# Kernel optimization log

Measured on AMD Instinct MI355X. Metric: run time of the kernel, lower is better.

The kernel has to match this reference:

```python
import jax, jax.numpy as jnp
import numpy as np

HEAD_NUM = 16
KEY_DIM = 64
EMBED = 1024
KV_OUT = HEAD_NUM * KEY_DIM  # 1024


def setup_inputs() -> dict:
    key = jax.random.key(0)
    ks = jax.random.split(key, 11)
    B, L, E = 2, 2048, EMBED
    scale = 0.02
    return {
        "query": jax.random.normal(ks[0], (B, L, E), jnp.float32),
        "key": jax.random.normal(ks[1], (B, L, E), jnp.float32),
        "value": jax.random.normal(ks[2], (B, L, E), jnp.float32),
        "W_Query": jax.random.normal(ks[3], (E, KV_OUT), jnp.float32) * scale,
        "W_Key": jax.random.normal(ks[4], (E, KV_OUT), jnp.float32) * scale,
        "W_Value": jax.random.normal(ks[5], (E, KV_OUT), jnp.float32) * scale,
        "W_Output": jax.random.normal(ks[6], (KV_OUT, E), jnp.float32) * scale,
        "B_Query": jnp.zeros((KV_OUT,), jnp.float32),
        "B_Key": jnp.zeros((KV_OUT,), jnp.float32),
        "B_Value": jnp.zeros((KV_OUT,), jnp.float32),
        "B_Output": jnp.zeros((E,), jnp.float32),
    }


def reference(query, key, value, W_Query, W_Key, W_Value, W_Output,
              B_Query, B_Key, B_Value, B_Output):
    B, Lq, E = query.shape
    Lk = key.shape[1]
    H, D = HEAD_NUM, KEY_DIM
    # QKV projections + bias
    q = query @ W_Query + B_Query            # [B, Lq, H*D]
    k = key @ W_Key + B_Key                  # [B, Lk, H*D]
    v = value @ W_Value + B_Value            # [B, Lk, H*D]
    # tf.split(axis=2) per head == reshape to [B, L, H, D]
    q = q.reshape(B, Lq, H, D)
    k = k.reshape(B, Lk, H, D)
    v = v.reshape(B, Lk, H, D)
    # scaled dot-product attention (no mask, dropout=0)
    scores = jnp.einsum("bqhd,bkhd->bhqk", q, k) / (D ** 0.5)
    probs = jax.nn.softmax(scores, axis=-1)
    out = jnp.einsum("bhqk,bkhd->bqhd", probs, v)  # [B, Lq, H, D]
    out = out.reshape(B, Lq, H * D)
    return out @ W_Output + B_Output
```

## Files before the change

### kernel.cpp

```cpp
#include <hip/hip_runtime.h>

using u16 = unsigned short;
using u32 = unsigned int;

typedef __attribute__((ext_vector_type(8))) short bf16x8;
typedef __attribute__((ext_vector_type(4))) float f32x4;
typedef __attribute__((ext_vector_type(4))) u32 u32x4;
typedef __attribute__((ext_vector_type(2))) u32 u32x2;
typedef __attribute__((ext_vector_type(4))) _Float16 f16x4;

#define MFMA_BF16_K32(a, b, c) __builtin_amdgcn_mfma_f32_16x16x32_bf16((a), (b), (c), 0, 0, 0)
#define MFMA_F16_K16(a, b, c) __builtin_amdgcn_mfma_f32_16x16x16f16((a), (b), (c), 0, 0, 0)

#define QSCALE 0.18033688011112042f

extern "C" __device__ float __ocml_native_exp2_f32(float);

__device__ __forceinline__ u16 f2bf(float f) {
  u32 u = __builtin_bit_cast(u32, f);
  return (u16)((u + 0x7fffu + ((u >> 16) & 1u)) >> 16);
}

__device__ __forceinline__ u32 pk_f16(float a, float b) {
  auto v = __builtin_amdgcn_cvt_pkrtz(a, b);
  return __builtin_bit_cast(u32, v);
}

__device__ __forceinline__ void load_lds16(const void* g, void* l) {
  __builtin_amdgcn_global_load_lds((__attribute__((address_space(1))) void*)g,
                                   (__attribute__((address_space(3))) void*)l,
                                   16, 0, 0);
}

__global__ __launch_bounds__(256) void cvt_all_kernel(
    const float* __restrict__ q, const float* __restrict__ k, const float* __restrict__ v,
    u16* __restrict__ oq, u16* __restrict__ ok, u16* __restrict__ ov,
    const float* __restrict__ w0, const float* __restrict__ w1,
    const float* __restrict__ w2, const float* __restrict__ w3,
    u16* __restrict__ d0, u16* __restrict__ d1,
    u16* __restrict__ d2, u16* __restrict__ d3) {
  const int id = blockIdx.x;
  const int tid = threadIdx.x;
  if (id < 6144) {
    const int z = id >> 11, bx = id & 2047;
    const float* s = z == 0 ? q : z == 1 ? k : v;
    u16* d = z == 0 ? oq : z == 1 ? ok : ov;
    int i = (bx * 256 + tid) * 8;
    f32x4 a = *(const f32x4*)(s + i);
    f32x4 b = *(const f32x4*)(s + i + 4);
    u32x4 o;
    o.x = (u32)f2bf(a.x) | ((u32)f2bf(a.y) << 16);
    o.y = (u32)f2bf(a.z) | ((u32)f2bf(a.w) << 16);
    o.z = (u32)f2bf(b.x) | ((u32)f2bf(b.y) << 16);
    o.w = (u32)f2bf(b.z) | ((u32)f2bf(b.w) << 16);
    *(u32x4*)(d + i) = o;
    return;
  }
  __shared__ float t[64][65];
  const int r0 = id - 6144;
  const int z = r0 >> 8, rr0 = r0 & 255;
  const int bx = rr0 & 15, by = rr0 >> 4;
  const float* src = z == 0 ? w0 : z == 1 ? w1 : z == 2 ? w2 : w3;
  u16* dst = z == 0 ? d0 : z == 1 ? d1 : z == 2 ? d2 : d3;
  const float scale = (z == 0) ? QSCALE : 1.0f;
  const int r = tid >> 4, c4 = (tid & 15) * 4;
#pragma unroll
  for (int i = 0; i < 4; ++i) {
    int row = r + i * 16;
    f32x4 vv = *(const f32x4*)(src + (by * 64 + row) * 1024 + bx * 64 + c4);
    t[row][c4 + 0] = vv.x;
    t[row][c4 + 1] = vv.y;
    t[row][c4 + 2] = vv.z;
    t[row][c4 + 3] = vv.w;
  }
  __syncthreads();
  const int rw = tid >> 2, cc = (tid & 3) * 16;
  alignas(16) u16 tmp[16];
#pragma unroll
  for (int j = 0; j < 16; ++j) tmp[j] = f2bf(t[cc + j][rw] * scale);
  u32x4* outp = (u32x4*)(dst + (bx * 64 + rw) * 1024 + by * 64 + cc);
  outp[0] = *(const u32x4*)&tmp[0];
  outp[1] = *(const u32x4*)&tmp[8];
}

__global__ __launch_bounds__(256) void gemm_qkv_kernel(
    const u16* __restrict__ x0, const u16* __restrict__ x1, const u16* __restrict__ x2,
    const u16* __restrict__ w0, const u16* __restrict__ w1, const u16* __restrict__ w2,
    const float* __restrict__ b0, const float* __restrict__ b1, const float* __restrict__ b2,
    u16* __restrict__ c0, u16* __restrict__ c1, u16* __restrict__ vt) {
  __shared__ u16 As[128 * 64];
  __shared__ u16 Bs[128 * 64];
  const int lid = blockIdx.x;
  const int xcd = lid & 7, rr = lid >> 3;
  const int nb = rr & 7, slot = rr >> 3;
  const int g = slot * 8 + xcd;
  const int z = g >> 5, m_idx = g & 31;
  const u16* A = z == 0 ? x0 : z == 1 ? x1 : x2;
  const u16* Bt = z == 0 ? w0 : z == 1 ? w1 : w2;
  const float* bias = z == 0 ? b0 : z == 1 ? b1 : b2;
  const float bscale = z == 0 ? QSCALE : 1.0f;
  const int tid = threadIdx.x;
  const int wave = tid >> 6, lane = tid & 63;
  const int l16 = lane & 15, quad = lane >> 4;
  const int l7 = l16 & 7;
  const int wm = wave >> 1, wn = wave & 1;
  const int m0 = m_idx * 128, n0 = nb * 128;

  f32x4 acc[4][4];
  const f32x4 zf = {0.f, 0.f, 0.f, 0.f};
#pragma unroll
  for (int i = 0; i < 4; ++i)
#pragma unroll
    for (int j = 0; j < 4; ++j) acc[i][j] = zf;

  for (int kb = 0; kb < 1024; kb += 64) {
#pragma unroll
    for (int t = 0; t < 4; ++t) {
      int c = wave * 256 + t * 64 + lane;
      int row = c >> 3, sc8 = (c & 7) ^ (row & 7);
      load_lds16(A + (m0 + row) * 1024 + kb + sc8 * 8, &As[(wave * 256 + t * 64) * 8]);
    }
#pragma unroll
    for (int t = 0; t < 4; ++t) {
      int c = wave * 256 + t * 64 + lane;
      int row = c >> 3, sc8 = (c & 7) ^ (row & 7);
      load_lds16(Bt + (n0 + row) * 1024 + kb + sc8 * 8, &Bs[(wave * 256 + t * 64) * 8]);
    }
    asm volatile("s_waitcnt vmcnt(0)" ::: "memory");
    __syncthreads();
#pragma unroll
    for (int ks = 0; ks < 2; ++ks) {
      const int sch = (ks * 4 + quad) ^ l7;
      bf16x8 af[4], bfv[4];
#pragma unroll
      for (int mt = 0; mt < 4; ++mt)
        af[mt] = *(const bf16x8*)&As[(wm * 64 + mt * 16 + l16) * 64 + sch * 8];
#pragma unroll
      for (int nt = 0; nt < 4; ++nt)
        bfv[nt] = *(const bf16x8*)&Bs[(wn * 64 + nt * 16 + l16) * 64 + sch * 8];
#pragma unroll
      for (int mt = 0; mt < 4; ++mt)
#pragma unroll
        for (int nt = 0; nt < 4; ++nt) acc[mt][nt] = MFMA_BF16_K32(af[mt], bfv[nt], acc[mt][nt]);
    }
    __syncthreads();
  }

  float bv[4];
#pragma unroll
  for (int nt = 0; nt < 4; ++nt) bv[nt] = bias[n0 + wn * 64 + nt * 16 + l16] * bscale;
  if (z != 2) {
    u16* C = z == 0 ? c0 : c1;
#pragma unroll
    for (int mt = 0; mt < 4; ++mt)
#pragma unroll
      for (int nt = 0; nt < 4; ++nt)
#pragma unroll
        for (int r = 0; r < 4; ++r) {
          int row = m0 + wm * 64 + mt * 16 + quad * 4 + r;
          int col = n0 + wn * 64 + nt * 16 + l16;
          C[row * 1024 + col] = f2bf(acc[mt][nt][r] + bv[nt]);
        }
  } else {
#pragma unroll
    for (int mt = 0; mt < 4; ++mt)
#pragma unroll
      for (int nt = 0; nt < 4; ++nt) {
        int kvb = m0 + wm * 64 + mt * 16 + quad * 4;
        int bb = kvb >> 11, kv = kvb & 2047;
        int col = n0 + wn * 64 + nt * 16 + l16;
        int h = col >> 6, dt = (col >> 4) & 3, ld = col & 15;
        int pair = bb * 16 + h;
        int kb2 = kv >> 7, chunk = (kv >> 4) & 7, qd = (kv >> 2) & 3;
        f16x4 hv;
#pragma unroll
        for (int r = 0; r < 4; ++r) hv[r] = (_Float16)(acc[mt][nt][r] + bv[nt]);
        u16* dst = vt + ((((pair * 16 + kb2) * 8 + chunk) * 4 + dt) * 256) + qd * 64 + ld * 4;
        *(f16x4*)dst = hv;
      }
  }
}

__global__ __launch_bounds__(256) void gemm_out_kernel(const u16* __restrict__ A,
                                                       const u16* __restrict__ Bt,
                                                       const float* __restrict__ bias,
                                                       float* __restrict__ C) {
  __shared__ u16 As[64 * 64];
  __shared__ u16 Bs[128 * 64];
  const int lid = blockIdx.x;
  const int xcd = lid & 7, rr = lid >> 3;
  const int nb = rr & 7, slot = rr >> 3;
  const int by = slot * 8 + xcd;
  const int tid = threadIdx.x;
  const int wave = tid >> 6, lane = tid & 63;
  const int l16 = lane & 15, quad = lane >> 4;
  const int l7 = l16 & 7;
  const int m0 = by * 64, n0 = nb * 128;

  f32x4 acc[4][2];
  const f32x4 zf = {0.f, 0.f, 0.f, 0.f};
#pragma unroll
  for (int i = 0; i < 4; ++i)
#pragma unroll
    for (int j = 0; j < 2; ++j) acc[i][j] = zf;

  for (int kb = 0; kb < 1024; kb += 64) {
#pragma unroll
    for (int t = 0; t < 2; ++t) {
      int c = wave * 128 + t * 64 + lane;
      int row = c >> 3, sc8 = (c & 7) ^ (row & 7);
      load_lds16(A + (m0 + row) * 1024 + kb + sc8 * 8, &As[(wave * 128 + t * 64) * 8]);
    }
#pragma unroll
    for (int t = 0; t < 4; ++t) {
      int c = wave * 256 + t * 64 + lane;
      int row = c >> 3, sc8 = (c & 7) ^ (row & 7);
      load_lds16(Bt + (n0 + row) * 1024 + kb + sc8 * 8, &Bs[(wave * 256 + t * 64) * 8]);
    }
    asm volatile("s_waitcnt vmcnt(0)" ::: "memory");
    __syncthreads();
#pragma unroll
    for (int ks = 0; ks < 2; ++ks) {
      const int sch = (ks * 4 + quad) ^ l7;
      bf16x8 af[4], bfv[2];
#pragma unroll
      for (int mt = 0; mt < 4; ++mt)
        af[mt] = *(const bf16x8*)&As[(mt * 16 + l16) * 64 + sch * 8];
#pragma unroll
      for (int nt = 0; nt < 2; ++nt)
        bfv[nt] = *(const bf16x8*)&Bs[(wave * 32 + nt * 16 + l16) * 64 + sch * 8];
#pragma unroll
      for (int mt = 0; mt < 4; ++mt)
#pragma unroll
        for (int nt = 0; nt < 2; ++nt) acc[mt][nt] = MFMA_BF16_K32(af[mt], bfv[nt], acc[mt][nt]);
    }
    __syncthreads();
  }

  float bv[2];
#pragma unroll
  for (int nt = 0; nt < 2; ++nt) bv[nt] = bias[n0 + wave * 32 + nt * 16 + l16];
#pragma unroll
  for (int mt = 0; mt < 4; ++mt)
#pragma unroll
    for (int nt = 0; nt < 2; ++nt)
#pragma unroll
      for (int r = 0; r < 4; ++r) {
        int row = m0 + mt * 16 + quad * 4 + r;
        int col = n0 + wave * 32 + nt * 16 + l16;
        C[row * 1024 + col] = acc[mt][nt][r] + bv[nt];
      }
}

__global__ __launch_bounds__(256, 2) void flash_kernel(const u16* __restrict__ Q,
                                                       const u16* __restrict__ K,
                                                       const u16* __restrict__ Vt,
                                                       u16* __restrict__ O) {
  __shared__ u16 k_lds[2][128 * 64];
  __shared__ float lred[4][64];
  __shared__ float lfin[64];
  const int tid = threadIdx.x;
  const int wave = tid >> 6, lane = tid & 63;
  const int l16 = lane & 15, quad = lane >> 4;
  const int l7 = l16 & 7;
  const int id = blockIdx.x;
  const int xcd = id & 7, slot = id >> 3;
  const int pair = xcd * 4 + (slot & 3);
  const int qb = slot >> 2;
  const int b = pair >> 4, h = pair & 15;
  const u16* Qh = Q + (b * 2048 + qb * 64) * 1024 + h * 64;
  const u16* Kh = K + b * 2048 * 1024 + h * 64;
  const u16* Vh = Vt + pair * 131072;

#pragma unroll
  for (int t = 0; t < 2; ++t) {
    int c = (t * 4 + wave) * 64 + lane;
    int row = c >> 3, sc8 = (c & 7) ^ (row & 7);
    load_lds16(Qh + row * 1024 + sc8 * 8, &k_lds[0][((t * 4 + wave) * 64) * 8]);
  }
  asm volatile("s_waitcnt vmcnt(0)" ::: "memory");
  __syncthreads();
  bf16x8 qf[4][2];
#pragma unroll
  for (int qn = 0; qn < 4; ++qn)
#pragma unroll
    for (int ks = 0; ks < 2; ++ks)
      qf[qn][ks] = *(const bf16x8*)&k_lds[0][(qn * 16 + l16) * 64 + (((ks * 4 + quad) ^ l7)) * 8];
  __syncthreads();

#pragma unroll
  for (int bufi = 0; bufi < 2; ++bufi) {
#pragma unroll
    for (int t = 0; t < 4; ++t) {
      int c = (t * 4 + wave) * 64 + lane;
      int row = c >> 3, sc8 = (c & 7) ^ (row & 7);
      load_lds16(Kh + (bufi * 128 + row) * 1024 + sc8 * 8,
                 &k_lds[bufi][((t * 4 + wave) * 64) * 8]);
    }
  }

  f32x4 o_acc[4][4];
  const f32x4 zf = {0.f, 0.f, 0.f, 0.f};
#pragma unroll
  for (int qn = 0; qn < 4; ++qn)
#pragma unroll
    for (int dt = 0; dt < 4; ++dt) o_acc[qn][dt] = zf;
  float lp[4] = {0.f, 0.f, 0.f, 0.f};

  for (int kb = 0; kb < 16; ++kb) {
    const int cur = kb & 1;
    if (kb == 0) asm volatile("s_waitcnt vmcnt(4)" ::: "memory");
    __builtin_amdgcn_s_barrier();
    asm volatile("" ::: "memory");

    const u16* vp = Vh + kb * 8192;
    f16x4 vreg[2][4];
#pragma unroll
    for (int c2 = 0; c2 < 2; ++c2) {
      const int chunk = wave * 2 + c2;
#pragma unroll
      for (int dt = 0; dt < 4; ++dt)
        vreg[c2][dt] = *(const f16x4*)(vp + (chunk * 4 + dt) * 256 + lane * 4);
    }

    union { u32 u[2]; f16x4 v; } pkv[2][4];
#pragma unroll
    for (int c2 = 0; c2 < 2; ++c2) {
      const int chunk = wave * 2 + c2;
      f32x4 s_acc[4];
#pragma unroll
      for (int qn = 0; qn < 4; ++qn) s_acc[qn] = zf;
#pragma unroll
      for (int ks = 0; ks < 2; ++ks) {
        bf16x8 kf =
            *(const bf16x8*)&k_lds[cur][(chunk * 16 + l16) * 64 + ((ks * 4 + quad) ^ l7) * 8];
        __builtin_amdgcn_s_setprio(1);
#pragma unroll
        for (int qn = 0; qn < 4; ++qn) s_acc[qn] = MFMA_BF16_K32(kf, qf[qn][ks], s_acc[qn]);
        __builtin_amdgcn_s_setprio(0);
      }
#pragma unroll
      for (int qn = 0; qn < 4; ++qn) {
        float e0 = __ocml_native_exp2_f32(s_acc[qn].x);
        float e1 = __ocml_native_exp2_f32(s_acc[qn].y);
        float e2 = __ocml_native_exp2_f32(s_acc[qn].z);
        float e3 = __ocml_native_exp2_f32(s_acc[qn].w);
        lp[qn] += (e0 + e1) + (e2 + e3);
        pkv[c2][qn].u[0] = pk_f16(e0, e1);
        pkv[c2][qn].u[1] = pk_f16(e2, e3);
      }
    }

    asm volatile("s_waitcnt lgkmcnt(0)" ::: "memory");
    __builtin_amdgcn_s_barrier();
    asm volatile("" ::: "memory");

    if (kb + 2 < 16) {
      const int kv0 = (kb + 2) * 128;
#pragma unroll
      for (int t = 0; t < 4; ++t) {
        int c = (t * 4 + wave) * 64 + lane;
        int row = c >> 3, sc8 = (c & 7) ^ (row & 7);
        load_lds16(Kh + (kv0 + row) * 1024 + sc8 * 8, &k_lds[cur][((t * 4 + wave) * 64) * 8]);
      }
    }
    if (kb < 14)
      asm volatile("s_waitcnt vmcnt(4)" ::: "memory");
    else
      asm volatile("s_waitcnt vmcnt(0)" ::: "memory");

#pragma unroll
    for (int c2 = 0; c2 < 2; ++c2) {
#pragma unroll
      for (int dt = 0; dt < 4; ++dt) {
        __builtin_amdgcn_s_setprio(1);
#pragma unroll
        for (int qn = 0; qn < 4; ++qn)
          o_acc[qn][dt] = MFMA_F16_K16(pkv[c2][qn].v, vreg[c2][dt], o_acc[qn][dt]);
        __builtin_amdgcn_s_setprio(0);
      }
    }
  }

#pragma unroll
  for (int qn = 0; qn < 4; ++qn) {
    lp[qn] += __shfl_xor(lp[qn], 16);
    lp[qn] += __shfl_xor(lp[qn], 32);
  }
  if (quad == 0) {
#pragma unroll
    for (int qn = 0; qn < 4; ++qn) lred[wave][qn * 16 + l16] = lp[qn];
  }
  float* bufA = (float*)&k_lds[0][0];
  float* bufB = (float*)&k_lds[1][0];
  if (wave == 1 || wave == 3) {
    float* buf = (wave == 1) ? bufA : bufB;
#pragma unroll
    for (int qm = 0; qm < 4; ++qm)
#pragma unroll
      for (int dt = 0; dt < 4; ++dt)
        *(f32x4*)&buf[(((qm * 4 + dt) * 4 + quad) * 16 + l16) * 4] = o_acc[qm][dt];
  }
  __syncthreads();
  if (tid < 64) lfin[tid] = lred[0][tid] + lred[1][tid] + lred[2][tid] + lred[3][tid];
  if (wave == 0 || wave == 2) {
    float* buf = (wave == 0) ? bufA : bufB;
#pragma unroll
    for (int qm = 0; qm < 4; ++qm)
#pragma unroll
      for (int dt = 0; dt < 4; ++dt)
        o_acc[qm][dt] += *(const f32x4*)&buf[(((qm * 4 + dt) * 4 + quad) * 16 + l16) * 4];
  }
  __syncthreads();
  if (wave == 2) {
#pragma unroll
    for (int qm = 0; qm < 4; ++qm)
#pragma unroll
      for (int dt = 0; dt < 4; ++dt)
        *(f32x4*)&bufA[(((qm * 4 + dt) * 4 + quad) * 16 + l16) * 4] = o_acc[qm][dt];
  }
  __syncthreads();
  if (wave == 0) {
#pragma unroll
    for (int qm = 0; qm < 4; ++qm)
#pragma unroll
      for (int dt = 0; dt < 4; ++dt)
        o_acc[qm][dt] += *(const f32x4*)&bufA[(((qm * 4 + dt) * 4 + quad) * 16 + l16) * 4];
#pragma unroll
    for (int qm = 0; qm < 4; ++qm)
#pragma unroll
      for (int r = 0; r < 4; ++r) {
        int qrow = qm * 16 + quad * 4 + r;
        float inv = 1.0f / lfin[qrow];
        int row = b * 2048 + qb * 64 + qrow;
#pragma unroll
        for (int dt = 0; dt < 4; ++dt)
          O[row * 1024 + h * 64 + dt * 16 + l16] = f2bf(o_acc[qm][dt][r] * inv);
      }
  }
}

extern "C" void kernel_launch(void* const* d_in, const int* in_sizes, int n_in,
                              void* d_out, int out_size, void* d_ws, size_t ws_size,
                              hipStream_t stream) {
  const float* q = (const float*)d_in[0];
  const float* k = (const float*)d_in[1];
  const float* v = (const float*)d_in[2];
  const float* Wq = (const float*)d_in[3];
  const float* Wk = (const float*)d_in[4];
  const float* Wv = (const float*)d_in[5];
  const float* Wo = (const float*)d_in[6];
  const float* Bq = (const float*)d_in[7];
  const float* Bk = (const float*)d_in[8];
  const float* Bv = (const float*)d_in[9];
  const float* Bo = (const float*)d_in[10];
  float* out = (float*)d_out;

  char* w = (char*)d_ws;
  const size_t MB = 1u << 20;
  u16* xq = (u16*)(w + 0 * MB);
  u16* xk = (u16*)(w + 8 * MB);
  u16* xv = (u16*)(w + 16 * MB);
  u16* wqt = (u16*)(w + 24 * MB);
  u16* wkt = (u16*)(w + 26 * MB);
  u16* wvt = (u16*)(w + 28 * MB);
  u16* wot = (u16*)(w + 30 * MB);
  u16* Qp = (u16*)(w + 32 * MB);
  u16* Kp = (u16*)(w + 40 * MB);
  u16* Vtr = (u16*)(w + 48 * MB);
  u16* At = (u16*)(w + 56 * MB);

  cvt_all_kernel<<<dim3(7168), 256, 0, stream>>>(q, k, v, xq, xk, xv,
                                                 Wq, Wk, Wv, Wo, wqt, wkt, wvt, wot);
  gemm_qkv_kernel<<<dim3(768), 256, 0, stream>>>(xq, xk, xv, wqt, wkt, wvt,
                                                 Bq, Bk, Bv, Qp, Kp, Vtr);
  flash_kernel<<<dim3(1024), 256, 0, stream>>>(Qp, Kp, Vtr, At);
  gemm_out_kernel<<<dim3(512), 256, 0, stream>>>(At, wot, Bo, out);
}
```

Before: 229.6 us.

## Prefetch V fragments one iteration ahead with double-buffered registers in flash loop

The flash attention loop now loads the V fragments for the next key block into a second register set while the current block is processed. The loop is unrolled by two via macros so the register buffers alternate, and the vmcnt waits are retuned to match. The s_setprio hints around the MFMAs are dropped. This aims to hide the global-memory latency of V loads behind the QK/exp work, at the cost of extra VGPRs, which could hurt occupancy under launch_bounds(256,2).

```diff
diff --git a/kernel.cpp b/kernel.cpp
--- a/kernel.cpp
+++ b/kernel.cpp
@@ -252,6 +252,66 @@
       }
 }
 
+union PU { u32 u[2]; f16x4 v; };
+
+#define QK_EXP(CUR, PKV)                                                          \
+  _Pragma("unroll") for (int c2 = 0; c2 < 2; ++c2) {                              \
+    const int chunk = wave * 2 + c2;                                              \
+    f32x4 s_acc[4];                                                               \
+    _Pragma("unroll") for (int qn = 0; qn < 4; ++qn) s_acc[qn] = zf;              \
+    _Pragma("unroll") for (int ks = 0; ks < 2; ++ks) {                            \
+      bf16x8 kf = *(const bf16x8*)&k_lds[CUR][(chunk * 16 + l16) * 64 +           \
+                                              ((ks * 4 + quad) ^ l7) * 8];        \
+      _Pragma("unroll") for (int qn = 0; qn < 4; ++qn)                            \
+        s_acc[qn] = MFMA_BF16_K32(kf, qf[qn][ks], s_acc[qn]);                     \
+    }                                                                             \
+    _Pragma("unroll") for (int qn = 0; qn < 4; ++qn) {                            \
+      float e0 = __ocml_native_exp2_f32(s_acc[qn].x);                             \
+      float e1 = __ocml_native_exp2_f32(s_acc[qn].y);                             \
+      float e2 = __ocml_native_exp2_f32(s_acc[qn].z);                             \
+      float e3 = __ocml_native_exp2_f32(s_acc[qn].w);                             \
+      lp[qn] += (e0 + e1) + (e2 + e3);                                            \
+      PKV[c2][qn].u[0] = pk_f16(e0, e1);                                          \
+      PKV[c2][qn].u[1] = pk_f16(e2, e3);                                          \
+    }                                                                             \
+  }
+
+#define FLASH_BODY(KB, CUR, VCUR, VNXT, PFV, PFK, WAIT)                           \
+  {                                                                               \
+    __builtin_amdgcn_s_barrier();                                                 \
+    asm volatile("" ::: "memory");                                                \
+    if (PFV) {                                                                    \
+      const u16* vp = Vh + ((KB) + 1) * 8192;                                     \
+      _Pragma("unroll") for (int c2 = 0; c2 < 2; ++c2)                            \
+        _Pragma("unroll") for (int dt = 0; dt < 4; ++dt)                          \
+          VNXT[c2][dt] =                                                          \
+              *(const f16x4*)(vp + ((wave * 2 + c2) * 4 + dt) * 256 + lane * 4);  \
+    }                                                                             \
+    PU pkv[2][4];                                                                 \
+    QK_EXP(CUR, pkv)                                                              \
+    asm volatile("s_waitcnt lgkmcnt(0)" ::: "memory");                            \
+    __builtin_amdgcn_s_barrier();                                                 \
+    asm volatile("" ::: "memory");                                                \
+    if (PFK) {                                                                    \
+      const int kv0 = ((KB) + 2) * 128;                                           \
+      _Pragma("unroll") for (int t = 0; t < 4; ++t) {                             \
+        int c = (t * 4 + wave) * 64 + lane;                                       \
+        int row = c >> 3, sc8 = (c & 7) ^ (row & 7);                              \
+        load_lds16(Kh + (kv0 + row) * 1024 + sc8 * 8,                             \
+                   &k_lds[CUR][((t * 4 + wave) * 64) * 8]);                       \
+      }                                                                           \
+    }                                                                             \
+    WAIT;                                                                         \
+    _Pragma("unroll") for (int c2 = 0; c2 < 2; ++c2)                              \
+      _Pragma("unroll") for (int dt = 0; dt < 4; ++dt)                            \
+        _Pragma("unroll") for (int qn = 0; qn < 4; ++qn)                          \
+          o_acc[qn][dt] = MFMA_F16_K16(pkv[c2][qn].v, VCUR[c2][dt], o_acc[qn][dt]); \
+  }
+
+#define W12 asm volatile("s_waitcnt vmcnt(12)" ::: "memory")
+#define W8 asm volatile("s_waitcnt vmcnt(8)" ::: "memory")
+#define W0 asm volatile("s_waitcnt vmcnt(0)" ::: "memory")
+
 __global__ __launch_bounds__(256, 2) void flash_kernel(const u16* __restrict__ Q,
                                                        const u16* __restrict__ K,
                                                        const u16* __restrict__ Vt,
@@ -289,15 +349,24 @@
   __syncthreads();
 
 #pragma unroll
-  for (int bufi = 0; bufi < 2; ++bufi) {
-#pragma unroll
-    for (int t = 0; t < 4; ++t) {
-      int c = (t * 4 + wave) * 64 + lane;
-      int row = c >> 3, sc8 = (c & 7) ^ (row & 7);
-      load_lds16(Kh + (bufi * 128 + row) * 1024 + sc8 * 8,
-                 &k_lds[bufi][((t * 4 + wave) * 64) * 8]);
-    }
-  }
+  for (int t = 0; t < 4; ++t) {
+    int c = (t * 4 + wave) * 64 + lane;
+    int row = c >> 3, sc8 = (c & 7) ^ (row & 7);
+    load_lds16(Kh + row * 1024 + sc8 * 8, &k_lds[0][((t * 4 + wave) * 64) * 8]);
+  }
+  f16x4 vregA[2][4], vregB[2][4];
+#pragma unroll
+  for (int c2 = 0; c2 < 2; ++c2)
+#pragma unroll
+    for (int dt = 0; dt < 4; ++dt)
+      vregA[c2][dt] = *(const f16x4*)(Vh + ((wave * 2 + c2) * 4 + dt) * 256 + lane * 4);
+#pragma unroll
+  for (int t = 0; t < 4; ++t) {
+    int c = (t * 4 + wave) * 64 + lane;
+    int row = c >> 3, sc8 = (c & 7) ^ (row & 7);
+    load_lds16(Kh + (128 + row) * 1024 + sc8 * 8, &k_lds[1][((t * 4 + wave) * 64) * 8]);
+  }
+  W12;
 
   f32x4 o_acc[4][4];
   const f32x4 zf = {0.f, 0.f, 0.f, 0.f};
@@ -307,80 +376,13 @@
     for (int dt = 0; dt < 4; ++dt) o_acc[qn][dt] = zf;
   float lp[4] = {0.f, 0.f, 0.f, 0.f};
 
-  for (int kb = 0; kb < 16; ++kb) {
-    const int cur = kb & 1;
-    if (kb == 0) asm volatile("s_waitcnt vmcnt(4)" ::: "memory");
-    __builtin_amdgcn_s_barrier();
-    asm volatile("" ::: "memory");
-
-    const u16* vp = Vh + kb * 8192;
-    f16x4 vreg[2][4];
-#pragma unroll
-    for (int c2 = 0; c2 < 2; ++c2) {
-      const int chunk = wave * 2 + c2;
-#pragma unroll
-      for (int dt = 0; dt < 4; ++dt)
-        vreg[c2][dt] = *(const f16x4*)(vp + (chunk * 4 + dt) * 256 + lane * 4);
-    }
-
-    union { u32 u[2]; f16x4 v; } pkv[2][4];
-#pragma unroll
-    for (int c2 = 0; c2 < 2; ++c2) {
-      const int chunk = wave * 2 + c2;
-      f32x4 s_acc[4];
-#pragma unroll
-      for (int qn = 0; qn < 4; ++qn) s_acc[qn] = zf;
-#pragma unroll
-      for (int ks = 0; ks < 2; ++ks) {
-        bf16x8 kf =
-            *(const bf16x8*)&k_lds[cur][(chunk * 16 + l16) * 64 + ((ks * 4 + quad) ^ l7) * 8];
-        __builtin_amdgcn_s_setprio(1);
-#pragma unroll
-        for (int qn = 0; qn < 4; ++qn) s_acc[qn] = MFMA_BF16_K32(kf, qf[qn][ks], s_acc[qn]);
-        __builtin_amdgcn_s_setprio(0);
-      }
-#pragma unroll
-      for (int qn = 0; qn < 4; ++qn) {
-        float e0 = __ocml_native_exp2_f32(s_acc[qn].x);
-        float e1 = __ocml_native_exp2_f32(s_acc[qn].y);
-        float e2 = __ocml_native_exp2_f32(s_acc[qn].z);
-        float e3 = __ocml_native_exp2_f32(s_acc[qn].w);
-        lp[qn] += (e0 + e1) + (e2 + e3);
-        pkv[c2][qn].u[0] = pk_f16(e0, e1);
-        pkv[c2][qn].u[1] = pk_f16(e2, e3);
-      }
-    }
-
-    asm volatile("s_waitcnt lgkmcnt(0)" ::: "memory");
-    __builtin_amdgcn_s_barrier();
-    asm volatile("" ::: "memory");
-
-    if (kb + 2 < 16) {
-      const int kv0 = (kb + 2) * 128;
-#pragma unroll
-      for (int t = 0; t < 4; ++t) {
-        int c = (t * 4 + wave) * 64 + lane;
-        int row = c >> 3, sc8 = (c & 7) ^ (row & 7);
-        load_lds16(Kh + (kv0 + row) * 1024 + sc8 * 8, &k_lds[cur][((t * 4 + wave) * 64) * 8]);
-      }
-    }
-    if (kb < 14)
-      asm volatile("s_waitcnt vmcnt(4)" ::: "memory");
-    else
-      asm volatile("s_waitcnt vmcnt(0)" ::: "memory");
-
-#pragma unroll
-    for (int c2 = 0; c2 < 2; ++c2) {
-#pragma unroll
-      for (int dt = 0; dt < 4; ++dt) {
-        __builtin_amdgcn_s_setprio(1);
-#pragma unroll
-        for (int qn = 0; qn < 4; ++qn)
-          o_acc[qn][dt] = MFMA_F16_K16(pkv[c2][qn].v, vreg[c2][dt], o_acc[qn][dt]);
-        __builtin_amdgcn_s_setprio(0);
-      }
-    }
-  }
+  for (int kb2 = 0; kb2 < 7; ++kb2) {
+    const int kb = kb2 * 2;
+    FLASH_BODY(kb, 0, vregA, vregB, true, true, W12);
+    FLASH_BODY(kb + 1, 1, vregB, vregA, true, true, W12);
+  }
+  FLASH_BODY(14, 0, vregA, vregB, true, false, W8);
+  FLASH_BODY(15, 1, vregB, vregA, false, false, W0);
 
 #pragma unroll
   for (int qn = 0; qn < 4; ++qn) {
```

Result: no change. 225.9 us (-1.6%).
